# Kernel tuning notes

Measured on AMD Instinct MI355X. Metric: run time of the kernel, lower is better.

## Reference

```python
import jax, jax.numpy as jnp
import numpy as np

N_NODES = 100000
N_EDGES = 1250000
D_FEAT = 64


def setup_inputs() -> dict:
    key = jax.random.key(0)
    kx, ke = jax.random.split(key)
    x = jax.random.normal(kx, (N_NODES, D_FEAT), dtype=jnp.float32)
    edge_index = jax.random.randint(ke, (2, N_EDGES), 0, N_NODES, dtype=jnp.int64)
    return {"x": x, "edge_index": edge_index}


def reference(x, edge_index):
    # propagate: scatter_nested gathers x[idxj] grouped by destination idxi
    # (a ragged per-node neighbor set); the module's sum_nested reduces each
    # group. Expressed densely and jit-ably as gather + segment-sum.
    idxi = edge_index[0, :]  # destination nodes
    idxj = edge_index[1, :]  # source nodes
    messages = x[idxj]  # [E, D] edge-level gather (memory-bound)
    out = jax.ops.segment_sum(messages, idxi, num_segments=N_NODES)  # [N, D]
    return out
```

## Files before the change

### kernel.cpp

```cpp
#include <hip/hip_runtime.h>

#define N_NODES 100000
#define N_EDGES 1250000
#define D_FEAT  64

#define NPB     256
#define NBINS   ((N_NODES + NPB - 1) / NPB)
#define BCAP    4096
#define EPB     4096
#define K1B     ((N_EDGES + EPB - 1) / EPB)
#define OVF_CAP 32768

__global__ __launch_bounds__(512) void k1_bin_kernel(
        const int* __restrict__ idxi, const int* __restrict__ idxj,
        int* __restrict__ gcursor, int* __restrict__ ovfcnt,
        int* __restrict__ ovf, int* __restrict__ binbuf) {
    __shared__ int hist[NBINS + 1];
    __shared__ int runstart[NBINS + 1];
    __shared__ int gbase[NBINS];
    __shared__ int cur[NBINS];
    __shared__ int staged[EPB];
    __shared__ unsigned short sbin[EPB];
    int t = threadIdx.x;
    if (t <= NBINS) hist[t] = 0;
    __syncthreads();

    int base = blockIdx.x * EPB;
    int n = N_EDGES - base; if (n > EPB) n = EPB;

    int d[8], s[8], bn[8];
#pragma unroll
    for (int j = 0; j < 8; ++j) {
        int i = t + j * 512;
        if (i < n) { d[j] = idxi[base + i]; s[j] = idxj[base + i]; }
        else       { d[j] = -1; s[j] = 0; }
    }
#pragma unroll
    for (int j = 0; j < 8; ++j) {
        bn[j] = (d[j] >= 0) ? (d[j] >> 8) : -1;
        if (bn[j] >= 0) atomicAdd(&hist[bn[j]], 1);
    }
    __syncthreads();

    if (t < 64) {
        int h[7];
        int sum = 0;
#pragma unroll
        for (int q = 0; q < 7; ++q) {
            int b = t * 7 + q;
            h[q] = (b < NBINS) ? hist[b] : 0;
            sum += h[q];
        }
        int inc = sum;
#pragma unroll
        for (int off = 1; off < 64; off <<= 1) {
            int u = __shfl_up(inc, off, 64);
            if (t >= off) inc += u;
        }
        int ex = inc - sum;
#pragma unroll
        for (int q = 0; q < 7; ++q) {
            int b = t * 7 + q;
            if (b < NBINS) runstart[b] = ex;
            ex += h[q];
        }
    }
    __syncthreads();

    if (t < NBINS) {
        int h = hist[t];
        gbase[t] = h ? atomicAdd(&gcursor[t], h) : 0;
        cur[t] = 0;
    }
    __syncthreads();

#pragma unroll
    for (int j = 0; j < 8; ++j) {
        if (bn[j] >= 0) {
            int idx = runstart[bn[j]] + atomicAdd(&cur[bn[j]], 1);
            staged[idx] = ((d[j] & 255) << 17) | s[j];
            sbin[idx] = (unsigned short)bn[j];
        }
    }
    __syncthreads();

    for (int i = t; i < n; i += 512) {
        int b = sbin[i];
        int p = staged[i];
        int tgt = gbase[b] + (i - runstart[b]);
        if (tgt < BCAP) {
            binbuf[b * BCAP + tgt] = p;
        } else {
            int op = atomicAdd(ovfcnt, 1);
            if (op < OVF_CAP) { ovf[2 * op] = b * NPB + (p >> 17); ovf[2 * op + 1] = p & 0x1FFFF; }
        }
    }
}

__global__ __launch_bounds__(1024) void k23_fused_kernel(
        const float* __restrict__ x, const int* __restrict__ gcursor,
        const int* __restrict__ binbuf, float* __restrict__ out) {
    __shared__ int cnt[NPB];
    __shared__ int excl[NPB];
    __shared__ int cur[NPB];
    __shared__ int srt[BCAP];
    int bin = blockIdx.x;
    int t = threadIdx.x;
    if (t < NPB) cnt[t] = 0;
    __syncthreads();

    int n = gcursor[bin];
    if (n > BCAP) n = BCAP;
    const int* src = binbuf + (size_t)bin * BCAP;

    int p[4];
#pragma unroll
    for (int j = 0; j < 4; ++j) {
        int i = t + j * 1024;
        p[j] = (i < n) ? src[i] : -1;
    }
#pragma unroll
    for (int j = 0; j < 4; ++j)
        if (p[j] >= 0) atomicAdd(&cnt[p[j] >> 17], 1);
    __syncthreads();

    if (t < 64) {
        int b0 = t * 4;
        int h0 = cnt[b0], h1 = cnt[b0 + 1], h2 = cnt[b0 + 2], h3 = cnt[b0 + 3];
        int s01 = h0 + h1;
        int sum = s01 + h2 + h3;
        int inc = sum;
#pragma unroll
        for (int off = 1; off < 64; off <<= 1) {
            int u = __shfl_up(inc, off, 64);
            if (t >= off) inc += u;
        }
        int ex = inc - sum;
        excl[b0]     = ex;
        excl[b0 + 1] = ex + h0;
        excl[b0 + 2] = ex + s01;
        excl[b0 + 3] = ex + s01 + h2;
        cur[b0] = 0; cur[b0 + 1] = 0; cur[b0 + 2] = 0; cur[b0 + 3] = 0;
    }
    __syncthreads();

#pragma unroll
    for (int j = 0; j < 4; ++j) {
        if (p[j] >= 0) {
            int dl = p[j] >> 17;
            int pos = excl[dl] + atomicAdd(&cur[dl], 1);
            srt[pos] = p[j] & 0x1FFFF;
        }
    }
    __syncthreads();

    int w = t >> 6, lane = t & 63;
    int sub = lane >> 4, c4 = lane & 15;
    const float4* xp = (const float4*)x;
#pragma unroll
    for (int i2 = 0; i2 < 4; ++i2) {
        int dl = w * 16 + sub * 4 + i2;
        int node = bin * NPB + dl;
        int k = excl[dl];
        int end = k + cnt[dl];
        float4 acc = make_float4(0.f, 0.f, 0.f, 0.f);
        for (; k + 4 <= end; k += 4) {
            int a0 = srt[k], a1 = srt[k + 1], a2 = srt[k + 2], a3 = srt[k + 3];
            float4 v0 = xp[(size_t)a0 * 16 + c4];
            float4 v1 = xp[(size_t)a1 * 16 + c4];
            float4 v2 = xp[(size_t)a2 * 16 + c4];
            float4 v3 = xp[(size_t)a3 * 16 + c4];
            acc.x += (v0.x + v1.x) + (v2.x + v3.x);
            acc.y += (v0.y + v1.y) + (v2.y + v3.y);
            acc.z += (v0.z + v1.z) + (v2.z + v3.z);
            acc.w += (v0.w + v1.w) + (v2.w + v3.w);
        }
        for (; k < end; ++k) {
            float4 v0 = xp[(size_t)srt[k] * 16 + c4];
            acc.x += v0.x; acc.y += v0.y; acc.z += v0.z; acc.w += v0.w;
        }
        if (node < N_NODES)
            ((float4*)out)[(size_t)node * 16 + c4] = acc;
    }
}

__global__ __launch_bounds__(256) void ovf_fixup_kernel(
        const float* __restrict__ x, const int* __restrict__ ovfcnt,
        const int* __restrict__ ovf, float* __restrict__ out) {
    int n = *ovfcnt;
    if (n > OVF_CAP) n = OVF_CAP;
    long long total = (long long)n * 16;
    long long stride = (long long)gridDim.x * blockDim.x;
    for (long long t = blockIdx.x * blockDim.x + threadIdx.x; t < total; t += stride) {
        int e  = (int)(t >> 4);
        int fo = ((int)t & 15) << 2;
        int d = ovf[2 * e];
        int s = ovf[2 * e + 1];
        const float4 v = *(const float4*)(x + (size_t)s * D_FEAT + fo);
        float* o = out + (size_t)d * D_FEAT + fo;
        atomicAdd(o + 0, v.x);
        atomicAdd(o + 1, v.y);
        atomicAdd(o + 2, v.z);
        atomicAdd(o + 3, v.w);
    }
}


__global__ __launch_bounds__(256) void zero_f4_kernel(float* __restrict__ out, int n4) {
    int i = blockIdx.x * blockDim.x + threadIdx.x;
    if (i < n4) ((float4*)out)[i] = make_float4(0.f, 0.f, 0.f, 0.f);
}

__global__ __launch_bounds__(256) void scatter_add_kernel(const float* __restrict__ x,
                                                          const int* __restrict__ idxi,
                                                          const int* __restrict__ idxj,
                                                          float* __restrict__ out) {
    int t = blockIdx.x * blockDim.x + threadIdx.x;
    int e = t >> 4;
    if (e >= N_EDGES) return;
    int fo = (t & 15) << 2;
    int dst = idxi[e];
    int src = idxj[e];
    const float4 v = *(const float4*)(x + (size_t)src * D_FEAT + fo);
    float* o = out + (size_t)dst * D_FEAT + fo;
    atomicAdd(o + 0, v.x);
    atomicAdd(o + 1, v.y);
    atomicAdd(o + 2, v.z);
    atomicAdd(o + 3, v.w);
}

extern "C" void kernel_launch(void* const* d_in, const int* in_sizes, int n_in,
                              void* d_out, int out_size, void* d_ws, size_t ws_size,
                              hipStream_t stream) {
    const float* x  = (const float*)d_in[0];
    const int*   ei = (const int*)d_in[1];
    const int*   idxi = ei;
    const int*   idxj = ei + N_EDGES;
    float* out = (float*)d_out;

    {
        size_t need = (512 + 16 + 2 * (size_t)OVF_CAP +
                       (size_t)NBINS * BCAP) * sizeof(int);
        if (ws_size >= need) {
            int* gcursor = (int*)d_ws;
            int* ovfcnt  = gcursor + 512;
            int* ovf     = ovfcnt + 16;
            int* binbuf  = ovf + 2 * OVF_CAP;

            hipMemsetAsync(gcursor, 0, (512 + 16) * sizeof(int), stream);
            k1_bin_kernel<<<K1B, 512, 0, stream>>>(idxi, idxj, gcursor, ovfcnt, ovf, binbuf);
            k23_fused_kernel<<<NBINS, 1024, 0, stream>>>(x, gcursor, binbuf, out);
            ovf_fixup_kernel<<<16, 256, 0, stream>>>(x, ovfcnt, ovf, out);
            return;
        }
    }

    int n4 = (N_NODES * D_FEAT) / 4;
    zero_f4_kernel<<<(n4 + 255) / 256, 256, 0, stream>>>(out, n4);
    long long total_threads = (long long)N_EDGES * 16;
    scatter_add_kernel<<<(int)((total_threads + 255) / 256), 256, 0, stream>>>(x, idxi, idxj, out);
}
```

Baseline: 136.4 us.

## Use 256 node bins to match CU count and fuse overflow fixup

Repartitions destination nodes into 256 bins of 392 nodes so the gather/reduce kernel runs one block per CU in a single wave, and enlarges per-block edge tiles and bin capacity accordingly. The separate overflow fixup kernel is removed and its work is folded into the tail of the fused kernel, where each block scans the overflow list for its own node range. This removes a launch and the partial second wave, at the cost of integer division during binning and more serial work per block.

```diff
diff --git a/kernel.cpp b/kernel.cpp
--- a/kernel.cpp
+++ b/kernel.cpp
@@ -4,10 +4,11 @@
 #define N_EDGES 1250000
 #define D_FEAT  64
 
-#define NPB     256
-#define NBINS   ((N_NODES + NPB - 1) / NPB)
-#define BCAP    4096
-#define EPB     4096
+#define NPB     392
+#define NBINS   256
+#define BCAP    6144
+#define EPB     5120
+#define EPT     10
 #define K1B     ((N_EDGES + EPB - 1) / EPB)
 #define OVF_CAP 32768
 
@@ -15,42 +16,38 @@
         const int* __restrict__ idxi, const int* __restrict__ idxj,
         int* __restrict__ gcursor, int* __restrict__ ovfcnt,
         int* __restrict__ ovf, int* __restrict__ binbuf) {
-    __shared__ int hist[NBINS + 1];
-    __shared__ int runstart[NBINS + 1];
+    __shared__ int hist[NBINS];
+    __shared__ int runstart[NBINS];
     __shared__ int gbase[NBINS];
     __shared__ int cur[NBINS];
     __shared__ int staged[EPB];
-    __shared__ unsigned short sbin[EPB];
+    __shared__ unsigned char sbin[EPB];
     int t = threadIdx.x;
-    if (t <= NBINS) hist[t] = 0;
+    if (t < NBINS) hist[t] = 0;
     __syncthreads();
 
     int base = blockIdx.x * EPB;
     int n = N_EDGES - base; if (n > EPB) n = EPB;
 
-    int d[8], s[8], bn[8];
-#pragma unroll
-    for (int j = 0; j < 8; ++j) {
+    int d[EPT], s[EPT], bn[EPT];
+#pragma unroll
+    for (int j = 0; j < EPT; ++j) {
         int i = t + j * 512;
         if (i < n) { d[j] = idxi[base + i]; s[j] = idxj[base + i]; }
         else       { d[j] = -1; s[j] = 0; }
     }
 #pragma unroll
-    for (int j = 0; j < 8; ++j) {
-        bn[j] = (d[j] >= 0) ? (d[j] >> 8) : -1;
+    for (int j = 0; j < EPT; ++j) {
+        bn[j] = (d[j] >= 0) ? (d[j] / NPB) : -1;
         if (bn[j] >= 0) atomicAdd(&hist[bn[j]], 1);
     }
     __syncthreads();
 
     if (t < 64) {
-        int h[7];
-        int sum = 0;
-#pragma unroll
-        for (int q = 0; q < 7; ++q) {
-            int b = t * 7 + q;
-            h[q] = (b < NBINS) ? hist[b] : 0;
-            sum += h[q];
-        }
+        int b0 = t * 4;
+        int h0 = hist[b0], h1 = hist[b0 + 1], h2 = hist[b0 + 2], h3 = hist[b0 + 3];
+        int s01 = h0 + h1;
+        int sum = s01 + h2 + h3;
         int inc = sum;
 #pragma unroll
         for (int off = 1; off < 64; off <<= 1) {
@@ -58,12 +55,10 @@
             if (t >= off) inc += u;
         }
         int ex = inc - sum;
-#pragma unroll
-        for (int q = 0; q < 7; ++q) {
-            int b = t * 7 + q;
-            if (b < NBINS) runstart[b] = ex;
-            ex += h[q];
-        }
+        runstart[b0]     = ex;
+        runstart[b0 + 1] = ex + h0;
+        runstart[b0 + 2] = ex + s01;
+        runstart[b0 + 3] = ex + s01 + h2;
     }
     __syncthreads();
 
@@ -75,11 +70,11 @@
     __syncthreads();
 
 #pragma unroll
-    for (int j = 0; j < 8; ++j) {
+    for (int j = 0; j < EPT; ++j) {
         if (bn[j] >= 0) {
             int idx = runstart[bn[j]] + atomicAdd(&cur[bn[j]], 1);
-            staged[idx] = ((d[j] & 255) << 17) | s[j];
-            sbin[idx] = (unsigned short)bn[j];
+            staged[idx] = ((d[j] - bn[j] * NPB) << 17) | s[j];
+            sbin[idx] = (unsigned char)bn[j];
         }
     }
     __syncthreads();
@@ -99,7 +94,8 @@
 
 __global__ __launch_bounds__(1024) void k23_fused_kernel(
         const float* __restrict__ x, const int* __restrict__ gcursor,
-        const int* __restrict__ binbuf, float* __restrict__ out) {
+        const int* __restrict__ binbuf, const int* __restrict__ ovfcnt,
+        const int* __restrict__ ovf, float* __restrict__ out) {
     __shared__ int cnt[NPB];
     __shared__ int excl[NPB];
     __shared__ int cur[NPB];
@@ -113,22 +109,26 @@
     if (n > BCAP) n = BCAP;
     const int* src = binbuf + (size_t)bin * BCAP;
 
-    int p[4];
-#pragma unroll
-    for (int j = 0; j < 4; ++j) {
+    int p[6];
+#pragma unroll
+    for (int j = 0; j < 6; ++j) {
         int i = t + j * 1024;
         p[j] = (i < n) ? src[i] : -1;
     }
 #pragma unroll
-    for (int j = 0; j < 4; ++j)
+    for (int j = 0; j < 6; ++j)
         if (p[j] >= 0) atomicAdd(&cnt[p[j] >> 17], 1);
     __syncthreads();
 
     if (t < 64) {
-        int b0 = t * 4;
-        int h0 = cnt[b0], h1 = cnt[b0 + 1], h2 = cnt[b0 + 2], h3 = cnt[b0 + 3];
-        int s01 = h0 + h1;
-        int sum = s01 + h2 + h3;
+        int h[7];
+        int sum = 0;
+#pragma unroll
+        for (int q = 0; q < 7; ++q) {
+            int b = t * 7 + q;
+            h[q] = (b < NPB) ? cnt[b] : 0;
+            sum += h[q];
+        }
         int inc = sum;
 #pragma unroll
         for (int off = 1; off < 64; off <<= 1) {
@@ -136,16 +136,17 @@
             if (t >= off) inc += u;
         }
         int ex = inc - sum;
-        excl[b0]     = ex;
-        excl[b0 + 1] = ex + h0;
-        excl[b0 + 2] = ex + s01;
-        excl[b0 + 3] = ex + s01 + h2;
-        cur[b0] = 0; cur[b0 + 1] = 0; cur[b0 + 2] = 0; cur[b0 + 3] = 0;
-    }
-    __syncthreads();
-
-#pragma unroll
-    for (int j = 0; j < 4; ++j) {
+#pragma unroll
+        for (int q = 0; q < 7; ++q) {
+            int b = t * 7 + q;
+            if (b < NPB) { excl[b] = ex; cur[b] = 0; }
+            ex += h[q];
+        }
+    }
+    __syncthreads();
+
+#pragma unroll
+    for (int j = 0; j < 6; ++j) {
         if (p[j] >= 0) {
             int dl = p[j] >> 17;
             int pos = excl[dl] + atomicAdd(&cur[dl], 1);
@@ -154,12 +155,11 @@
     }
     __syncthreads();
 
-    int w = t >> 6, lane = t & 63;
-    int sub = lane >> 4, c4 = lane & 15;
+    int sg = t >> 4, c4 = t & 15;
     const float4* xp = (const float4*)x;
-#pragma unroll
-    for (int i2 = 0; i2 < 4; ++i2) {
-        int dl = w * 16 + sub * 4 + i2;
+    for (int i2 = 0; i2 < 7; ++i2) {
+        int dl = sg + (i2 << 6);
+        if (dl >= NPB) break;
         int node = bin * NPB + dl;
         int k = excl[dl];
         int end = k + cnt[dl];
@@ -182,26 +182,22 @@
         if (node < N_NODES)
             ((float4*)out)[(size_t)node * 16 + c4] = acc;
     }
-}
-
-__global__ __launch_bounds__(256) void ovf_fixup_kernel(
-        const float* __restrict__ x, const int* __restrict__ ovfcnt,
-        const int* __restrict__ ovf, float* __restrict__ out) {
-    int n = *ovfcnt;
-    if (n > OVF_CAP) n = OVF_CAP;
-    long long total = (long long)n * 16;
-    long long stride = (long long)gridDim.x * blockDim.x;
-    for (long long t = blockIdx.x * blockDim.x + threadIdx.x; t < total; t += stride) {
-        int e  = (int)(t >> 4);
-        int fo = ((int)t & 15) << 2;
-        int d = ovf[2 * e];
-        int s = ovf[2 * e + 1];
-        const float4 v = *(const float4*)(x + (size_t)s * D_FEAT + fo);
-        float* o = out + (size_t)d * D_FEAT + fo;
-        atomicAdd(o + 0, v.x);
-        atomicAdd(o + 1, v.y);
-        atomicAdd(o + 2, v.z);
-        atomicAdd(o + 3, v.w);
+
+    __syncthreads();
+    int novf = *ovfcnt;
+    if (novf > 0) {
+        __threadfence();
+        if (novf > OVF_CAP) novf = OVF_CAP;
+        int lo = bin * NPB;
+        for (int e = t; e < novf; e += 1024) {
+            int dnode = ovf[2 * e];
+            if ((unsigned)(dnode - lo) < NPB && dnode < N_NODES) {
+                int snode = ovf[2 * e + 1];
+                const float* vsrc = x + (size_t)snode * D_FEAT;
+                float* o = out + (size_t)dnode * D_FEAT;
+                for (int f = 0; f < D_FEAT; ++f) atomicAdd(o + f, vsrc[f]);
+            }
+        }
     }
 }
 
@@ -239,18 +235,17 @@
     float* out = (float*)d_out;
 
     {
-        size_t need = (512 + 16 + 2 * (size_t)OVF_CAP +
+        size_t need = (256 + 16 + 2 * (size_t)OVF_CAP +
                        (size_t)NBINS * BCAP) * sizeof(int);
         if (ws_size >= need) {
             int* gcursor = (int*)d_ws;
-            int* ovfcnt  = gcursor + 512;
+            int* ovfcnt  = gcursor + 256;
             int* ovf     = ovfcnt + 16;
             int* binbuf  = ovf + 2 * OVF_CAP;
 
-            hipMemsetAsync(gcursor, 0, (512 + 16) * sizeof(int), stream);
+            hipMemsetAsync(gcursor, 0, (256 + 16) * sizeof(int), stream);
             k1_bin_kernel<<<K1B, 512, 0, stream>>>(idxi, idxj, gcursor, ovfcnt, ovf, binbuf);
-            k23_fused_kernel<<<NBINS, 1024, 0, stream>>>(x, gcursor, binbuf, out);
-            ovf_fixup_kernel<<<16, 256, 0, stream>>>(x, ovfcnt, ovf, out);
+            k23_fused_kernel<<<NBINS, 1024, 0, stream>>>(x, gcursor, binbuf, ovfcnt, ovf, out);
             return;
         }
     }
```

Measured after the change: 132.6 us. 2.8% less time.
